# Kernel optimization log

Measured on AMD Instinct MI355X. Metric: run time of the kernel, lower is better.

The kernel has to match this reference:

```python
import jax, jax.numpy as jnp
import numpy as np

H = 2048          # hidden_size
E = 16            # n_routed_experts
K = 4             # num_experts_per_tok
I = 1408          # moe_intermediate_size
SH_I = 2 * I      # shared experts intermediate (n_shared_experts * moe_intermediate_size)
B, S = 1, 1024


def setup_inputs() -> dict:
    key = jax.random.key(0)
    ks = jax.random.split(key, 9)
    sc_h = 1.0 / np.sqrt(H)
    sc_i = 1.0 / np.sqrt(I)
    return {
        "hidden_states": jax.random.normal(ks[0], (B, S, H), dtype=jnp.float32),
        "w_gate": jax.random.normal(ks[1], (E, H), dtype=jnp.float32) * sc_h,
        "wg": jax.random.normal(ks[2], (E, H, I), dtype=jnp.float32) * sc_h,  # gate_proj per expert
        "wu": jax.random.normal(ks[3], (E, H, I), dtype=jnp.float32) * sc_h,  # up_proj per expert
        "wd": jax.random.normal(ks[4], (E, I, H), dtype=jnp.float32) * sc_i,  # down_proj per expert
        "sg": jax.random.normal(ks[5], (H, SH_I), dtype=jnp.float32) * sc_h,  # shared gate_proj
        "su": jax.random.normal(ks[6], (H, SH_I), dtype=jnp.float32) * sc_h,  # shared up_proj
        "sd": jax.random.normal(ks[7], (SH_I, H), dtype=jnp.float32) * (1.0 / np.sqrt(SH_I)),
    }


def reference(hidden_states, w_gate, wg, wu, wd, sg, su, sd):
    b, s, h = hidden_states.shape
    x = hidden_states.reshape(-1, h)                      # [T, H]
    T = x.shape[0]

    # --- router: softmax (fp32) -> topk -> scatter-add weights into [T, E] ---
    logits = x @ w_gate.T                                 # [T, E]
    probs = jax.nn.softmax(logits.astype(jnp.float32), axis=-1)
    top_w, top_i = jax.lax.top_k(probs, K)                # [T, K]
    routing_weight = jnp.zeros((T, E), dtype=probs.dtype)
    routing_weight = routing_weight.at[jnp.arange(T)[:, None], top_i].add(top_w)  # scatter_add_

    # --- routed experts (grouped SwiGLU MLPs), weighted combine ---
    g = jnp.einsum('th,ehi->tei', x, wg)                  # [T, E, I]
    u = jnp.einsum('th,ehi->tei', x, wu)
    act = jax.nn.silu(g) * u                              # [T, E, I]
    routed = jnp.einsum('te,tei,eih->th', routing_weight, act, wd)  # [T, H]

    # --- shared experts (always on) ---
    shared = (jax.nn.silu(x @ sg) * (x @ su)) @ sd        # [T, H]

    out = (routed + shared).astype(hidden_states.dtype)
    return out.reshape(b, s, h)
```

## Files before the change

kernel.cpp:

```cpp
#include <hip/hip_runtime.h>
#include <hip/hip_bf16.h>
#include <stdint.h>

#define T_NUM 1024
#define H_DIM 2048
#define E_NUM 16
#define TOPK 4
#define I_DIM 1408
#define SHI_DIM 2816

typedef __attribute__((ext_vector_type(4))) float f32x4;
typedef __attribute__((ext_vector_type(8))) short bf16x8;
typedef __attribute__((ext_vector_type(4))) short s16x4;

static __device__ __forceinline__ short f2bf(float f) {
    __hip_bfloat16 h = __float2bfloat16(f);
    return __builtin_bit_cast(short, h);
}
static __device__ __forceinline__ float bf2f(short s) {
    return __bfloat162float(__builtin_bit_cast(__hip_bfloat16, s));
}

__global__ void router_kernel(const float* __restrict__ x, const float* __restrict__ wgate,
                              int* __restrict__ top_e, float* __restrict__ top_w,
                              short* __restrict__ xb) {
    const int t = blockIdx.x;
    const int tid = threadIdx.x;
    __shared__ float xsh[H_DIM];
    const float* xr = x + (size_t)t * H_DIM;
    for (int h = tid; h < H_DIM; h += 256) xsh[h] = xr[h];
    __syncthreads();

    {
        short v[8];
        #pragma unroll
        for (int i = 0; i < 8; ++i) v[i] = f2bf(xsh[tid * 8 + i]);
        *reinterpret_cast<bf16x8*>(xb + (size_t)t * H_DIM + tid * 8) = *(bf16x8*)v;
    }

    const int e = tid >> 4;
    const int j = tid & 15;
    const float* wr = wgate + (size_t)e * H_DIM;
    float acc = 0.f;
    for (int h = j; h < H_DIM; h += 16) acc += xsh[h] * wr[h];
    #pragma unroll
    for (int m = 8; m >= 1; m >>= 1) acc += __shfl_down(acc, m, 16);

    __shared__ float logits[E_NUM];
    if (j == 0) logits[e] = acc;
    __syncthreads();

    if (tid == 0) {
        float mx = logits[0];
        #pragma unroll
        for (int i = 1; i < E_NUM; ++i) mx = fmaxf(mx, logits[i]);
        float p[E_NUM]; float s = 0.f;
        #pragma unroll
        for (int i = 0; i < E_NUM; ++i) { p[i] = expf(logits[i] - mx); s += p[i]; }
        const float inv = 1.f / s;
        #pragma unroll
        for (int i = 0; i < E_NUM; ++i) p[i] *= inv;
        for (int k = 0; k < TOPK; ++k) {
            float best = -1.f; int bi = 0;
            #pragma unroll
            for (int i = 0; i < E_NUM; ++i) if (p[i] > best) { best = p[i]; bi = i; }
            top_e[t * TOPK + k] = bi;
            top_w[t * TOPK + k] = best;
            p[bi] = -2.f;
        }
    }
}

__global__ void perm_kernel(const int* __restrict__ top_e,
                            int* __restrict__ offs, int* __restrict__ perm) {
    __shared__ int cnt[256][E_NUM];
    __shared__ int base[E_NUM];
    const int tid = threadIdx.x;
    int c[E_NUM];
    #pragma unroll
    for (int i = 0; i < E_NUM; ++i) c[i] = 0;
    for (int s = tid * 16; s < tid * 16 + 16; ++s) c[top_e[s]]++;
    #pragma unroll
    for (int i = 0; i < E_NUM; ++i) cnt[tid][i] = c[i];
    __syncthreads();
    if (tid < E_NUM) {
        int run = 0;
        for (int b = 0; b < 256; ++b) { int v = cnt[b][tid]; cnt[b][tid] = run; run += v; }
        base[tid] = run;
    }
    __syncthreads();
    if (tid == 0) {
        int run = 0;
        for (int e2 = 0; e2 < E_NUM; ++e2) { int v = base[e2]; base[e2] = run; offs[e2] = run; run += v; }
        offs[E_NUM] = run;
    }
    __syncthreads();
    int run[E_NUM];
    #pragma unroll
    for (int i = 0; i < E_NUM; ++i) run[i] = base[i] + cnt[tid][i];
    for (int s = tid * 16; s < tid * 16 + 16; ++s) {
        int e2 = top_e[s];
        perm[run[e2]++] = s;
    }
}

__global__ void swiglu_kernel(const short* __restrict__ g, const short* __restrict__ u,
                              short* __restrict__ act, int n8) {
    const int i = blockIdx.x * 256 + threadIdx.x;
    if (i >= n8) return;
    bf16x8 gv = *reinterpret_cast<const bf16x8*>(g + (size_t)i * 8);
    bf16x8 uv = *reinterpret_cast<const bf16x8*>(u + (size_t)i * 8);
    short o[8];
    #pragma unroll
    for (int j = 0; j < 8; ++j) {
        float gf = bf2f(gv[j]);
        float uf = bf2f(uv[j]);
        o[j] = f2bf(gf / (1.f + __expf(-gf)) * uf);
    }
    *reinterpret_cast<bf16x8*>(act + (size_t)i * 8) = *(bf16x8*)o;
}

__global__ void combine_kernel(const short* __restrict__ dr, float* __restrict__ out) {
    const int i = blockIdx.x * 256 + threadIdx.x;
    const int t = i >> 8;
    const int h8 = (i & 255) * 8;
    float s[8];
    f32x4 o0 = *reinterpret_cast<const f32x4*>(out + (size_t)t * H_DIM + h8);
    f32x4 o1 = *reinterpret_cast<const f32x4*>(out + (size_t)t * H_DIM + h8 + 4);
    #pragma unroll
    for (int j = 0; j < 4; ++j) { s[j] = o0[j]; s[4 + j] = o1[j]; }
    #pragma unroll
    for (int k = 0; k < TOPK; ++k) {
        bf16x8 v = *reinterpret_cast<const bf16x8*>(dr + ((size_t)(t * TOPK + k)) * H_DIM + h8);
        #pragma unroll
        for (int j = 0; j < 8; ++j) s[j] += bf2f(v[j]);
    }
    f32x4 r0 = { s[0], s[1], s[2], s[3] };
    f32x4 r1 = { s[4], s[5], s[6], s[7] };
    *reinterpret_cast<f32x4*>(out + (size_t)t * H_DIM + h8) = r0;
    *reinterpret_cast<f32x4*>(out + (size_t)t * H_DIM + h8 + 4) = r1;
}

template<int MODE>
__global__ __launch_bounds__(256, 4) void gemm_n64(
    const short* __restrict__ A, int lda, int Kdim,
    const float* __restrict__ B1g, const float* __restrict__ B2g, int ldb,
    void* __restrict__ Out1v, void* __restrict__ Out2v, int ldo,
    const int* __restrict__ perm, const int* __restrict__ offs,
    const float* __restrict__ top_w, int nmt, int nnt, int nsplit)
{
    constexpr int KP = 40;
    __shared__ short As[2][128 * KP];
    __shared__ short Bs[2][64 * KP];
    __shared__ int   rows_a[128];
    __shared__ int   rows_o[128];
    __shared__ float w_m[128];

    const int tid = threadIdx.x;

    int wgid = blockIdx.x;
    {
        const int nwg = gridDim.x;
        const int qq = nwg >> 3, rr = nwg & 7;
        const int xcd = wgid & 7, lin = wgid >> 3;
        wgid = (xcd < rr ? xcd * (qq + 1) : rr * (qq + 1) + (xcd - rr) * qq) + lin;
    }
    const int mt  = wgid % nmt;
    const int ntt = (wgid / nmt) % nnt;
    const int e   = wgid / (nmt * nnt);

    int off = 0, cnt = T_NUM;
    const float* B1 = B1g;
    const float* B2 = B2g;
    if constexpr (MODE == 0) {
        off = offs[e]; cnt = offs[e + 1] - off;
        if (mt * 128 >= cnt) return;
        B1 = B1g + (size_t)e * H_DIM * I_DIM;
        B2 = B2g + (size_t)e * H_DIM * I_DIM;
    }
    if constexpr (MODE == 2) {
        off = offs[e]; cnt = offs[e + 1] - off;
        if (mt * 128 >= cnt) return;
        B1 = B1g + (size_t)e * I_DIM * H_DIM;
    }
    const float* Bsel = (ntt < nsplit) ? B1 : B2;
    const int ncol = (ntt % nsplit) * 64;

    if (tid < 128) {
        const int gm = mt * 128 + tid;
        if constexpr (MODE == 0) {
            int s = perm[off + (gm < cnt ? gm : cnt - 1)];
            rows_a[tid] = s >> 2; rows_o[tid] = s; w_m[tid] = 1.f;
        } else if constexpr (MODE == 2) {
            int s = perm[off + (gm < cnt ? gm : cnt - 1)];
            rows_a[tid] = s; rows_o[tid] = s; w_m[tid] = top_w[s];
        } else {
            rows_a[tid] = gm; rows_o[tid] = gm; w_m[tid] = 1.f;
        }
    }
    __syncthreads();

    int raReg[2];
    #pragma unroll
    for (int it = 0; it < 2; ++it) raReg[it] = rows_a[it * 64 + (tid >> 2)];

    bf16x8 aReg[2];
    float  bReg[8];

    const int bn = tid & 63;
    const int bkb = (tid >> 6) * 8;

    auto gload = [&](int kt) {
        const int k0 = kt * 32;
        #pragma unroll
        for (int it = 0; it < 2; ++it) {
            const int q = it * 256 + tid;
            const int ko = (q & 3) * 8;
            aReg[it] = *reinterpret_cast<const bf16x8*>(A + (size_t)raReg[it] * lda + k0 + ko);
        }
        const float* p1 = Bsel + (size_t)(k0 + bkb) * ldb + ncol + bn;
        #pragma unroll
        for (int dk = 0; dk < 8; ++dk) bReg[dk] = p1[(size_t)dk * ldb];
    };

    auto swrite = [&](int buf) {
        #pragma unroll
        for (int it = 0; it < 2; ++it) {
            const int q = it * 256 + tid;
            const int m = q >> 2, ko = (q & 3) * 8;
            *reinterpret_cast<bf16x8*>(&As[buf][m * KP + ko]) = aReg[it];
        }
        s16x4 v0 = { f2bf(bReg[0]), f2bf(bReg[1]), f2bf(bReg[2]), f2bf(bReg[3]) };
        s16x4 v1 = { f2bf(bReg[4]), f2bf(bReg[5]), f2bf(bReg[6]), f2bf(bReg[7]) };
        *reinterpret_cast<s16x4*>(&Bs[buf][bn * KP + bkb]) = v0;
        *reinterpret_cast<s16x4*>(&Bs[buf][bn * KP + bkb + 4]) = v1;
    };

    f32x4 acc[4][2];
    #pragma unroll
    for (int i = 0; i < 4; ++i)
        #pragma unroll
        for (int j = 0; j < 2; ++j) acc[i][j] = (f32x4)0.f;

    const int lane = tid & 63;
    const int wr = (tid >> 7), wc = (tid >> 6) & 1;
    const int lrow = lane & 15;
    const int lko = (lane >> 4) * 8;

    auto compute = [&](int buf) {
        bf16x8 af[4];
        #pragma unroll
        for (int mi = 0; mi < 4; ++mi)
            af[mi] = *reinterpret_cast<const bf16x8*>(&As[buf][(wr * 64 + mi * 16 + lrow) * KP + lko]);
        #pragma unroll
        for (int ni = 0; ni < 2; ++ni) {
            bf16x8 bfr = *reinterpret_cast<const bf16x8*>(&Bs[buf][(wc * 32 + ni * 16 + lrow) * KP + lko]);
            #pragma unroll
            for (int mi = 0; mi < 4; ++mi)
                acc[mi][ni] = __builtin_amdgcn_mfma_f32_16x16x32_bf16(af[mi], bfr, acc[mi][ni], 0, 0, 0);
        }
    };

    const int NK = Kdim / 32;
    gload(0);
    int cur = 0;
    for (int kt = 0; kt < NK; ++kt) {
        swrite(cur);
        __syncthreads();
        if (kt + 1 < NK) gload(kt + 1);
        compute(cur);
        cur ^= 1;
    }

    #pragma unroll
    for (int mi = 0; mi < 4; ++mi) {
        #pragma unroll
        for (int j = 0; j < 4; ++j) {
            const int ml = wr * 64 + mi * 16 + (lane >> 4) * 4 + j;
            const int gm = mt * 128 + ml;
            if constexpr (MODE == 0 || MODE == 2) { if (gm >= cnt) continue; }
            const int orow = (MODE == 0 || MODE == 2) ? rows_o[ml] : gm;
            const float wsc = w_m[ml];
            #pragma unroll
            for (int ni = 0; ni < 2; ++ni) {
                const int n = ncol + wc * 32 + ni * 16 + (lane & 15);
                const float v = acc[mi][ni][j];
                if constexpr (MODE == 0 || MODE == 1) {
                    short* o = (short*)((ntt < nsplit) ? Out1v : Out2v);
                    o[(size_t)orow * ldo + n] = f2bf(v);
                } else if constexpr (MODE == 2) {
                    ((short*)Out1v)[(size_t)orow * ldo + n] = f2bf(v * wsc);
                } else {
                    ((float*)Out1v)[(size_t)orow * ldo + n] = v;
                }
            }
        }
    }
}

extern "C" void kernel_launch(void* const* d_in, const int* in_sizes, int n_in,
                              void* d_out, int out_size, void* d_ws, size_t ws_size,
                              hipStream_t stream) {
    const float* x     = (const float*)d_in[0];
    const float* wgate = (const float*)d_in[1];
    const float* wg    = (const float*)d_in[2];
    const float* wu    = (const float*)d_in[3];
    const float* wd    = (const float*)d_in[4];
    const float* sg    = (const float*)d_in[5];
    const float* su    = (const float*)d_in[6];
    const float* sd    = (const float*)d_in[7];
    float* out = (float*)d_out;

    uintptr_t p = (uintptr_t)d_ws;
    auto alloc = [&](size_t bytes) {
        p = (p + 255) & ~(uintptr_t)255;
        void* r = (void*)p; p += bytes; return r;
    };
    int*   top_e = (int*)alloc((size_t)T_NUM * TOPK * sizeof(int));
    float* top_w = (float*)alloc((size_t)T_NUM * TOPK * sizeof(float));
    int*   offs  = (int*)alloc((E_NUM + 1) * sizeof(int));
    int*   perm  = (int*)alloc((size_t)T_NUM * TOPK * sizeof(int));
    short* xb    = (short*)alloc((size_t)T_NUM * H_DIM * 2);
    short* g_r   = (short*)alloc((size_t)T_NUM * TOPK * I_DIM * 2);
    short* u_r   = (short*)alloc((size_t)T_NUM * TOPK * I_DIM * 2);
    short* act_r = (short*)alloc((size_t)T_NUM * TOPK * I_DIM * 2);
    short* g_s   = (short*)alloc((size_t)T_NUM * SHI_DIM * 2);
    short* u_s   = (short*)alloc((size_t)T_NUM * SHI_DIM * 2);
    short* act_s = (short*)alloc((size_t)T_NUM * SHI_DIM * 2);
    short* dr    = (short*)alloc((size_t)T_NUM * TOPK * H_DIM * 2);

    router_kernel<<<T_NUM, 256, 0, stream>>>(x, wgate, top_e, top_w, xb);
    perm_kernel<<<1, 256, 0, stream>>>(top_e, offs, perm);

    const int nmtT = T_NUM / 128;
    const int nnI  = I_DIM / 64;
    const int nnH  = H_DIM / 64;
    const int nnS  = SHI_DIM / 64;

    gemm_n64<1><<<nmtT * (2 * nnS), 256, 0, stream>>>(
        xb, H_DIM, H_DIM, sg, su, SHI_DIM, g_s, u_s, SHI_DIM,
        nullptr, nullptr, nullptr, nmtT, 2 * nnS, nnS);
    swiglu_kernel<<<(T_NUM * SHI_DIM / 8 + 255) / 256, 256, 0, stream>>>(
        g_s, u_s, act_s, T_NUM * SHI_DIM / 8);
    gemm_n64<3><<<nmtT * nnH, 256, 0, stream>>>(
        act_s, SHI_DIM, SHI_DIM, sd, nullptr, H_DIM, out, nullptr, H_DIM,
        nullptr, nullptr, nullptr, nmtT, nnH, nnH);

    gemm_n64<0><<<nmtT * (2 * nnI) * E_NUM, 256, 0, stream>>>(
        xb, H_DIM, H_DIM, wg, wu, I_DIM, g_r, u_r, I_DIM,
        perm, offs, nullptr, nmtT, 2 * nnI, nnI);
    swiglu_kernel<<<(T_NUM * TOPK * I_DIM / 8 + 255) / 256, 256, 0, stream>>>(
        g_r, u_r, act_r, T_NUM * TOPK * I_DIM / 8);
    gemm_n64<2><<<nmtT * nnH * E_NUM, 256, 0, stream>>>(
        act_r, I_DIM, I_DIM, wd, nullptr, H_DIM, dr, nullptr, H_DIM,
        perm, offs, top_w, nmtT, nnH, nnH);
    combine_kernel<<<T_NUM * H_DIM / 8 / 256, 256, 0, stream>>>(dr, out);
}
```

Before: 577.5 us.

## Use direct global-to-LDS loads with a three-stage ring in grouped GEMMs

Replaces the register-staged, double-buffered GEMM main loop with asynchronous global_load_lds transfers into a three-slot LDS ring, synchronised with vmcnt waits and a single barrier per K step. The A tile is XOR-swizzled to avoid LDS bank conflicts and drops its padding. The B weights now stay fp32 in LDS and are converted to bf16 at fragment-load time. The aim is to hide global memory latency and drop the VGPR round-trip, at the cost of more LDS per block (lower occupancy bound) and repeated B conversions in every wave.

```diff
diff --git a/kernel.cpp b/kernel.cpp
--- a/kernel.cpp
+++ b/kernel.cpp
@@ -19,6 +19,17 @@
 }
 static __device__ __forceinline__ float bf2f(short s) {
     return __bfloat162float(__builtin_bit_cast(__hip_bfloat16, s));
+}
+
+static __device__ __forceinline__ void gllA16(const short* g, const short* l) {
+    __builtin_amdgcn_global_load_lds(
+        (const __attribute__((address_space(1))) void*)g,
+        (__attribute__((address_space(3))) void*)l, 16, 0, 0);
+}
+static __device__ __forceinline__ void gllB16(const float* g, const float* l) {
+    __builtin_amdgcn_global_load_lds(
+        (const __attribute__((address_space(1))) void*)g,
+        (__attribute__((address_space(3))) void*)l, 16, 0, 0);
 }
 
 __global__ void router_kernel(const float* __restrict__ x, const float* __restrict__ wgate,
@@ -142,16 +153,15 @@
 }
 
 template<int MODE>
-__global__ __launch_bounds__(256, 4) void gemm_n64(
+__global__ __launch_bounds__(256, 3) void gemm_ring(
     const short* __restrict__ A, int lda, int Kdim,
     const float* __restrict__ B1g, const float* __restrict__ B2g, int ldb,
     void* __restrict__ Out1v, void* __restrict__ Out2v, int ldo,
     const int* __restrict__ perm, const int* __restrict__ offs,
     const float* __restrict__ top_w, int nmt, int nnt, int nsplit)
 {
-    constexpr int KP = 40;
-    __shared__ short As[2][128 * KP];
-    __shared__ short Bs[2][64 * KP];
+    __shared__ __align__(16) short As[3][128 * 32];
+    __shared__ __align__(16) float Bsf[3][32 * 64];
     __shared__ int   rows_a[128];
     __shared__ int   rows_o[128];
     __shared__ float w_m[128];
@@ -204,36 +214,22 @@
     #pragma unroll
     for (int it = 0; it < 2; ++it) raReg[it] = rows_a[it * 64 + (tid >> 2)];
 
-    bf16x8 aReg[2];
-    float  bReg[8];
-
-    const int bn = tid & 63;
-    const int bkb = (tid >> 6) * 8;
-
-    auto gload = [&](int kt) {
+    const int bk0 = tid >> 4,          const_bn0 = 0;
+    const int bn4a = (tid & 15) * 4;
+    const int bk1 = (tid + 256) >> 4;
+    const int bn4b = ((tid + 256) & 15) * 4;
+
+    auto stage = [&](int slot, int kt) {
         const int k0 = kt * 32;
         #pragma unroll
         for (int it = 0; it < 2; ++it) {
             const int q = it * 256 + tid;
-            const int ko = (q & 3) * 8;
-            aReg[it] = *reinterpret_cast<const bf16x8*>(A + (size_t)raReg[it] * lda + k0 + ko);
-        }
-        const float* p1 = Bsel + (size_t)(k0 + bkb) * ldb + ncol + bn;
-        #pragma unroll
-        for (int dk = 0; dk < 8; ++dk) bReg[dk] = p1[(size_t)dk * ldb];
-    };
-
-    auto swrite = [&](int buf) {
-        #pragma unroll
-        for (int it = 0; it < 2; ++it) {
-            const int q = it * 256 + tid;
-            const int m = q >> 2, ko = (q & 3) * 8;
-            *reinterpret_cast<bf16x8*>(&As[buf][m * KP + ko]) = aReg[it];
-        }
-        s16x4 v0 = { f2bf(bReg[0]), f2bf(bReg[1]), f2bf(bReg[2]), f2bf(bReg[3]) };
-        s16x4 v1 = { f2bf(bReg[4]), f2bf(bReg[5]), f2bf(bReg[6]), f2bf(bReg[7]) };
-        *reinterpret_cast<s16x4*>(&Bs[buf][bn * KP + bkb]) = v0;
-        *reinterpret_cast<s16x4*>(&Bs[buf][bn * KP + bkb + 4]) = v1;
+            const int m = q >> 2;
+            const int c = ((q & 3) ^ ((m >> 1) & 3)) * 8;
+            gllA16(A + (size_t)raReg[it] * lda + k0 + c, &As[slot][q * 8]);
+        }
+        gllB16(Bsel + (size_t)(k0 + bk0) * ldb + ncol + bn4a, &Bsf[slot][bk0 * 64 + bn4a]);
+        gllB16(Bsel + (size_t)(k0 + bk1) * ldb + ncol + bn4b, &Bsf[slot][bk1 * 64 + bn4b]);
     };
 
     f32x4 acc[4][2];
@@ -246,15 +242,20 @@
     const int wr = (tid >> 7), wc = (tid >> 6) & 1;
     const int lrow = lane & 15;
     const int lko = (lane >> 4) * 8;
-
-    auto compute = [&](int buf) {
+    const int cswz = (((lane >> 4) ^ ((lrow >> 1) & 3)) * 8);
+
+    auto compute = [&](int slot) {
         bf16x8 af[4];
         #pragma unroll
         for (int mi = 0; mi < 4; ++mi)
-            af[mi] = *reinterpret_cast<const bf16x8*>(&As[buf][(wr * 64 + mi * 16 + lrow) * KP + lko]);
+            af[mi] = *reinterpret_cast<const bf16x8*>(&As[slot][(wr * 64 + mi * 16 + lrow) * 32 + cswz]);
         #pragma unroll
         for (int ni = 0; ni < 2; ++ni) {
-            bf16x8 bfr = *reinterpret_cast<const bf16x8*>(&Bs[buf][(wc * 32 + ni * 16 + lrow) * KP + lko]);
+            const int n = wc * 32 + ni * 16 + lrow;
+            bf16x8 bfr;
+            #pragma unroll
+            for (int kk = 0; kk < 8; ++kk)
+                bfr[kk] = f2bf(Bsf[slot][(lko + kk) * 64 + n]);
             #pragma unroll
             for (int mi = 0; mi < 4; ++mi)
                 acc[mi][ni] = __builtin_amdgcn_mfma_f32_16x16x32_bf16(af[mi], bfr, acc[mi][ni], 0, 0, 0);
@@ -262,14 +263,19 @@
     };
 
     const int NK = Kdim / 32;
-    gload(0);
-    int cur = 0;
-    for (int kt = 0; kt < NK; ++kt) {
-        swrite(cur);
-        __syncthreads();
-        if (kt + 1 < NK) gload(kt + 1);
-        compute(cur);
-        cur ^= 1;
+
+    stage(0, 0);
+    stage(1, 1);
+    for (int t = 0; t < NK; ++t) {
+        if (t + 1 < NK) {
+            asm volatile("s_waitcnt vmcnt(4)" ::: "memory");
+        } else {
+            asm volatile("s_waitcnt vmcnt(0)" ::: "memory");
+        }
+        __builtin_amdgcn_sched_barrier(0);
+        __builtin_amdgcn_s_barrier();
+        compute(t % 3);
+        if (t + 2 < NK) stage((t + 2) % 3, t + 2);
     }
 
     #pragma unroll
@@ -337,21 +343,21 @@
     const int nnH  = H_DIM / 64;
     const int nnS  = SHI_DIM / 64;
 
-    gemm_n64<1><<<nmtT * (2 * nnS), 256, 0, stream>>>(
+    gemm_ring<1><<<nmtT * (2 * nnS), 256, 0, stream>>>(
         xb, H_DIM, H_DIM, sg, su, SHI_DIM, g_s, u_s, SHI_DIM,
         nullptr, nullptr, nullptr, nmtT, 2 * nnS, nnS);
     swiglu_kernel<<<(T_NUM * SHI_DIM / 8 + 255) / 256, 256, 0, stream>>>(
         g_s, u_s, act_s, T_NUM * SHI_DIM / 8);
-    gemm_n64<3><<<nmtT * nnH, 256, 0, stream>>>(
+    gemm_ring<3><<<nmtT * nnH, 256, 0, stream>>>(
         act_s, SHI_DIM, SHI_DIM, sd, nullptr, H_DIM, out, nullptr, H_DIM,
         nullptr, nullptr, nullptr, nmtT, nnH, nnH);
 
-    gemm_n64<0><<<nmtT * (2 * nnI) * E_NUM, 256, 0, stream>>>(
+    gemm_ring<0><<<nmtT * (2 * nnI) * E_NUM, 256, 0, stream>>>(
         xb, H_DIM, H_DIM, wg, wu, I_DIM, g_r, u_r, I_DIM,
         perm, offs, nullptr, nmtT, 2 * nnI, nnI);
     swiglu_kernel<<<(T_NUM * TOPK * I_DIM / 8 + 255) / 256, 256, 0, stream>>>(
         g_r, u_r, act_r, T_NUM * TOPK * I_DIM / 8);
-    gemm_n64<2><<<nmtT * nnH * E_NUM, 256, 0, stream>>>(
+    gemm_ring<2><<<nmtT * nnH * E_NUM, 256, 0, stream>>>(
         act_r, I_DIM, I_DIM, wd, nullptr, H_DIM, dr, nullptr, H_DIM,
         perm, offs, top_w, nmtT, nnH, nnH);
     combine_kernel<<<T_NUM * H_DIM / 8 / 256, 256, 0, stream>>>(dr, out);
```

New measurement: 593.9 us. +2.8%, slower.

## Replace LDS-tiled GEMM with single-wave register-direct MFMA kernel

Applied to the files above, without the earlier changes.

Rewrites the grouped GEMM as a one-wave workgroup computing a 32x64 tile. Operands are loaded straight from global memory into MFMA registers, with no shared memory staging or barriers. This removes LDS traffic and synchronization and gives finer-grained tiles for ragged expert token counts. In exchange, each weight tile is reused by 4x fewer rows, so global weight traffic rises substantially. Software double buffering is also lost.

```diff
diff --git a/kernel.cpp b/kernel.cpp
--- a/kernel.cpp
+++ b/kernel.cpp
@@ -11,7 +11,6 @@
 
 typedef __attribute__((ext_vector_type(4))) float f32x4;
 typedef __attribute__((ext_vector_type(8))) short bf16x8;
-typedef __attribute__((ext_vector_type(4))) short s16x4;
 
 static __device__ __forceinline__ short f2bf(float f) {
     __hip_bfloat16 h = __float2bfloat16(f);
@@ -142,21 +141,19 @@
 }
 
 template<int MODE>
-__global__ __launch_bounds__(256, 4) void gemm_n64(
-    const short* __restrict__ A, int lda, int Kdim,
-    const float* __restrict__ B1g, const float* __restrict__ B2g, int ldb,
-    void* __restrict__ Out1v, void* __restrict__ Out2v, int ldo,
+__global__ __launch_bounds__(64) void gemm_wave(
+    const short* __restrict__ A,
+    const float* __restrict__ B1g, const float* __restrict__ B2g,
+    void* __restrict__ Out1v, void* __restrict__ Out2v,
     const int* __restrict__ perm, const int* __restrict__ offs,
     const float* __restrict__ top_w, int nmt, int nnt, int nsplit)
 {
-    constexpr int KP = 40;
-    __shared__ short As[2][128 * KP];
-    __shared__ short Bs[2][64 * KP];
-    __shared__ int   rows_a[128];
-    __shared__ int   rows_o[128];
-    __shared__ float w_m[128];
-
-    const int tid = threadIdx.x;
+    constexpr int KD  = (MODE == 0 || MODE == 1) ? H_DIM : (MODE == 2 ? I_DIM : SHI_DIM);
+    constexpr int LDB = (MODE == 0) ? I_DIM : (MODE == 1) ? SHI_DIM : H_DIM;
+    constexpr int LDO = LDB;
+    constexpr int NK  = KD / 32;
+
+    const int lane = threadIdx.x;
 
     int wgid = blockIdx.x;
     {
@@ -174,124 +171,96 @@
     const float* B2 = B2g;
     if constexpr (MODE == 0) {
         off = offs[e]; cnt = offs[e + 1] - off;
-        if (mt * 128 >= cnt) return;
+        if (mt * 32 >= cnt) return;
         B1 = B1g + (size_t)e * H_DIM * I_DIM;
         B2 = B2g + (size_t)e * H_DIM * I_DIM;
     }
     if constexpr (MODE == 2) {
         off = offs[e]; cnt = offs[e + 1] - off;
-        if (mt * 128 >= cnt) return;
+        if (mt * 32 >= cnt) return;
         B1 = B1g + (size_t)e * I_DIM * H_DIM;
     }
     const float* Bsel = (ntt < nsplit) ? B1 : B2;
     const int ncol = (ntt % nsplit) * 64;
 
-    if (tid < 128) {
-        const int gm = mt * 128 + tid;
+    const short* Ap0;
+    const short* Ap1;
+    {
+        int gm0 = mt * 32 + (lane & 15);
+        int gm1 = gm0 + 16;
+        int ra0, ra1;
         if constexpr (MODE == 0) {
-            int s = perm[off + (gm < cnt ? gm : cnt - 1)];
-            rows_a[tid] = s >> 2; rows_o[tid] = s; w_m[tid] = 1.f;
+            int s0 = perm[off + (gm0 < cnt ? gm0 : cnt - 1)];
+            int s1 = perm[off + (gm1 < cnt ? gm1 : cnt - 1)];
+            ra0 = s0 >> 2; ra1 = s1 >> 2;
         } else if constexpr (MODE == 2) {
-            int s = perm[off + (gm < cnt ? gm : cnt - 1)];
-            rows_a[tid] = s; rows_o[tid] = s; w_m[tid] = top_w[s];
+            ra0 = perm[off + (gm0 < cnt ? gm0 : cnt - 1)];
+            ra1 = perm[off + (gm1 < cnt ? gm1 : cnt - 1)];
         } else {
-            rows_a[tid] = gm; rows_o[tid] = gm; w_m[tid] = 1.f;
+            ra0 = gm0; ra1 = gm1;
         }
-    }
-    __syncthreads();
-
-    int raReg[2];
-    #pragma unroll
-    for (int it = 0; it < 2; ++it) raReg[it] = rows_a[it * 64 + (tid >> 2)];
-
-    bf16x8 aReg[2];
-    float  bReg[8];
-
-    const int bn = tid & 63;
-    const int bkb = (tid >> 6) * 8;
-
-    auto gload = [&](int kt) {
+        Ap0 = A + (size_t)ra0 * KD;
+        Ap1 = A + (size_t)ra1 * KD;
+    }
+
+    const int koff = (lane >> 4) * 8;
+    const float* Bp = Bsel + (size_t)koff * LDB + ncol + (lane & 15);
+
+    f32x4 acc[2][4];
+    #pragma unroll
+    for (int i = 0; i < 2; ++i)
+        #pragma unroll
+        for (int j = 0; j < 4; ++j) acc[i][j] = (f32x4)0.f;
+
+    for (int kt = 0; kt < NK; ++kt) {
         const int k0 = kt * 32;
-        #pragma unroll
-        for (int it = 0; it < 2; ++it) {
-            const int q = it * 256 + tid;
-            const int ko = (q & 3) * 8;
-            aReg[it] = *reinterpret_cast<const bf16x8*>(A + (size_t)raReg[it] * lda + k0 + ko);
+        bf16x8 a0 = *reinterpret_cast<const bf16x8*>(Ap0 + k0 + koff);
+        bf16x8 a1 = *reinterpret_cast<const bf16x8*>(Ap1 + k0 + koff);
+        const float* bp = Bp + (size_t)k0 * LDB;
+        bf16x8 b0, b1, b2, b3;
+        #pragma unroll
+        for (int j = 0; j < 8; ++j) {
+            const float* r = bp + (size_t)j * LDB;
+            b0[j] = f2bf(r[0]);
+            b1[j] = f2bf(r[16]);
+            b2[j] = f2bf(r[32]);
+            b3[j] = f2bf(r[48]);
         }
-        const float* p1 = Bsel + (size_t)(k0 + bkb) * ldb + ncol + bn;
-        #pragma unroll
-        for (int dk = 0; dk < 8; ++dk) bReg[dk] = p1[(size_t)dk * ldb];
-    };
-
-    auto swrite = [&](int buf) {
-        #pragma unroll
-        for (int it = 0; it < 2; ++it) {
-            const int q = it * 256 + tid;
-            const int m = q >> 2, ko = (q & 3) * 8;
-            *reinterpret_cast<bf16x8*>(&As[buf][m * KP + ko]) = aReg[it];
-        }
-        s16x4 v0 = { f2bf(bReg[0]), f2bf(bReg[1]), f2bf(bReg[2]), f2bf(bReg[3]) };
-        s16x4 v1 = { f2bf(bReg[4]), f2bf(bReg[5]), f2bf(bReg[6]), f2bf(bReg[7]) };
-        *reinterpret_cast<s16x4*>(&Bs[buf][bn * KP + bkb]) = v0;
-        *reinterpret_cast<s16x4*>(&Bs[buf][bn * KP + bkb + 4]) = v1;
-    };
-
-    f32x4 acc[4][2];
-    #pragma unroll
-    for (int i = 0; i < 4; ++i)
-        #pragma unroll
-        for (int j = 0; j < 2; ++j) acc[i][j] = (f32x4)0.f;
-
-    const int lane = tid & 63;
-    const int wr = (tid >> 7), wc = (tid >> 6) & 1;
-    const int lrow = lane & 15;
-    const int lko = (lane >> 4) * 8;
-
-    auto compute = [&](int buf) {
-        bf16x8 af[4];
-        #pragma unroll
-        for (int mi = 0; mi < 4; ++mi)
-            af[mi] = *reinterpret_cast<const bf16x8*>(&As[buf][(wr * 64 + mi * 16 + lrow) * KP + lko]);
-        #pragma unroll
-        for (int ni = 0; ni < 2; ++ni) {
-            bf16x8 bfr = *reinterpret_cast<const bf16x8*>(&Bs[buf][(wc * 32 + ni * 16 + lrow) * KP + lko]);
+        acc[0][0] = __builtin_amdgcn_mfma_f32_16x16x32_bf16(a0, b0, acc[0][0], 0, 0, 0);
+        acc[1][0] = __builtin_amdgcn_mfma_f32_16x16x32_bf16(a1, b0, acc[1][0], 0, 0, 0);
+        acc[0][1] = __builtin_amdgcn_mfma_f32_16x16x32_bf16(a0, b1, acc[0][1], 0, 0, 0);
+        acc[1][1] = __builtin_amdgcn_mfma_f32_16x16x32_bf16(a1, b1, acc[1][1], 0, 0, 0);
+        acc[0][2] = __builtin_amdgcn_mfma_f32_16x16x32_bf16(a0, b2, acc[0][2], 0, 0, 0);
+        acc[1][2] = __builtin_amdgcn_mfma_f32_16x16x32_bf16(a1, b2, acc[1][2], 0, 0, 0);
+        acc[0][3] = __builtin_amdgcn_mfma_f32_16x16x32_bf16(a0, b3, acc[0][3], 0, 0, 0);
+        acc[1][3] = __builtin_amdgcn_mfma_f32_16x16x32_bf16(a1, b3, acc[1][3], 0, 0, 0);
+    }
+
+    #pragma unroll
+    for (int mi = 0; mi < 2; ++mi) {
+        #pragma unroll
+        for (int j = 0; j < 4; ++j) {
+            const int r = mt * 32 + mi * 16 + (lane >> 4) * 4 + j;
+            if constexpr (MODE == 0 || MODE == 2) { if (r >= cnt) continue; }
+            int orow; float w = 1.f;
+            if constexpr (MODE == 0) {
+                orow = perm[off + r];
+            } else if constexpr (MODE == 2) {
+                int s = perm[off + r]; orow = s; w = top_w[s];
+            } else {
+                orow = r;
+            }
             #pragma unroll
-            for (int mi = 0; mi < 4; ++mi)
-                acc[mi][ni] = __builtin_amdgcn_mfma_f32_16x16x32_bf16(af[mi], bfr, acc[mi][ni], 0, 0, 0);
-        }
-    };
-
-    const int NK = Kdim / 32;
-    gload(0);
-    int cur = 0;
-    for (int kt = 0; kt < NK; ++kt) {
-        swrite(cur);
-        __syncthreads();
-        if (kt + 1 < NK) gload(kt + 1);
-        compute(cur);
-        cur ^= 1;
-    }
-
-    #pragma unroll
-    for (int mi = 0; mi < 4; ++mi) {
-        #pragma unroll
-        for (int j = 0; j < 4; ++j) {
-            const int ml = wr * 64 + mi * 16 + (lane >> 4) * 4 + j;
-            const int gm = mt * 128 + ml;
-            if constexpr (MODE == 0 || MODE == 2) { if (gm >= cnt) continue; }
-            const int orow = (MODE == 0 || MODE == 2) ? rows_o[ml] : gm;
-            const float wsc = w_m[ml];
-            #pragma unroll
-            for (int ni = 0; ni < 2; ++ni) {
-                const int n = ncol + wc * 32 + ni * 16 + (lane & 15);
-                const float v = acc[mi][ni][j];
+            for (int nt2 = 0; nt2 < 4; ++nt2) {
+                const int n = ncol + nt2 * 16 + (lane & 15);
+                const float v = acc[mi][nt2][j];
                 if constexpr (MODE == 0 || MODE == 1) {
                     short* o = (short*)((ntt < nsplit) ? Out1v : Out2v);
-                    o[(size_t)orow * ldo + n] = f2bf(v);
+                    o[(size_t)orow * LDO + n] = f2bf(v);
                 } else if constexpr (MODE == 2) {
-                    ((short*)Out1v)[(size_t)orow * ldo + n] = f2bf(v * wsc);
+                    ((short*)Out1v)[(size_t)orow * LDO + n] = f2bf(v * w);
                 } else {
-                    ((float*)Out1v)[(size_t)orow * ldo + n] = v;
+                    ((float*)Out1v)[(size_t)orow * LDO + n] = v;
                 }
             }
         }
@@ -332,27 +301,24 @@
     router_kernel<<<T_NUM, 256, 0, stream>>>(x, wgate, top_e, top_w, xb);
     perm_kernel<<<1, 256, 0, stream>>>(top_e, offs, perm);
 
-    const int nmtT = T_NUM / 128;
+    const int nmtS = T_NUM / 32;
+    const int nmtR = T_NUM / 32;
     const int nnI  = I_DIM / 64;
     const int nnH  = H_DIM / 64;
     const int nnS  = SHI_DIM / 64;
 
-    gemm_n64<1><<<nmtT * (2 * nnS), 256, 0, stream>>>(
-        xb, H_DIM, H_DIM, sg, su, SHI_DIM, g_s, u_s, SHI_DIM,
-        nullptr, nullptr, nullptr, nmtT, 2 * nnS, nnS);
+    gemm_wave<1><<<nmtS * (2 * nnS), 64, 0, stream>>>(
+        xb, sg, su, g_s, u_s, nullptr, nullptr, nullptr, nmtS, 2 * nnS, nnS);
     swiglu_kernel<<<(T_NUM * SHI_DIM / 8 + 255) / 256, 256, 0, stream>>>(
         g_s, u_s, act_s, T_NUM * SHI_DIM / 8);
-    gemm_n64<3><<<nmtT * nnH, 256, 0, stream>>>(
-        act_s, SHI_DIM, SHI_DIM, sd, nullptr, H_DIM, out, nullptr, H_DIM,
-        nullptr, nullptr, nullptr, nmtT, nnH, nnH);
-
-    gemm_n64<0><<<nmtT * (2 * nnI) * E_NUM, 256, 0, stream>>>(
-        xb, H_DIM, H_DIM, wg, wu, I_DIM, g_r, u_r, I_DIM,
-        perm, offs, nullptr, nmtT, 2 * nnI, nnI);
+    gemm_wave<3><<<nmtS * nnH, 64, 0, stream>>>(
+        act_s, sd, nullptr, out, nullptr, nullptr, nullptr, nullptr, nmtS, nnH, nnH);
+
+    gemm_wave<0><<<nmtR * (2 * nnI) * E_NUM, 64, 0, stream>>>(
+        xb, wg, wu, g_r, u_r, perm, offs, nullptr, nmtR, 2 * nnI, nnI);
     swiglu_kernel<<<(T_NUM * TOPK * I_DIM / 8 + 255) / 256, 256, 0, stream>>>(
         g_r, u_r, act_r, T_NUM * TOPK * I_DIM / 8);
-    gemm_n64<2><<<nmtT * nnH * E_NUM, 256, 0, stream>>>(
-        act_r, I_DIM, I_DIM, wd, nullptr, H_DIM, dr, nullptr, H_DIM,
-        perm, offs, top_w, nmtT, nnH, nnH);
+    gemm_wave<2><<<nmtR * nnH * E_NUM, 64, 0, stream>>>(
+        act_r, wd, nullptr, dr, nullptr, perm, offs, top_w, nmtR, nnH, nnH);
     combine_kernel<<<T_NUM * H_DIM / 8 / 256, 256, 0, stream>>>(dr, out);
 }
```

New measurement: 828.4 us. 43.4% more time.
